# Kernel optimization log

Hardware: AMD Instinct MI355X
Metric: run time of the kernel (lower is better)

Reference implementation:

```python
import jax, jax.numpy as jnp
import numpy as np

NC = 16
NP_ = 2_000_000
Z_OFFSET = 50.0  # keep points well in front of every camera (stable 1/z)


def setup_inputs() -> dict:
    key = jax.random.key(0)
    k1, k2, k3, k4, k5 = jax.random.split(key, 5)
    pt3d = jax.random.normal(k1, (3, NP_), dtype=jnp.float32)
    R = jax.random.normal(k2, (NC, 3, 3), dtype=jnp.float32) * 0.3
    t = jax.random.normal(k3, (NC, 3), dtype=jnp.float32)
    t = t.at[:, 2].add(Z_OFFSET)
    f = jax.random.uniform(k4, (NC, 2), dtype=jnp.float32, minval=500.0, maxval=1500.0)
    c = jax.random.normal(k5, (NC, 2), dtype=jnp.float32) * 10.0
    mask = jnp.ones((NC, NP_), dtype=jnp.int32)  # full visibility (fixed output shape)
    return {"pt3d": pt3d, "R": R, "t": t, "f": f, "c": c, "mask": mask}


def reference(pt3d, R, t, f, c, mask):
    # Camera-frame points for every camera: Xc[n] = R[n] @ pt3d + t[n]  -> (Nc, 3, Np)
    Xc = jnp.einsum('nij,jp->nip', R, pt3d) + t[:, :, None]
    # Pinhole projection: (u, v) = f * (x/z, y/z) + c  -> (Nc, 2, Np)
    uv = Xc[:, :2, :] / Xc[:, 2:3, :] * f[:, :, None] + c[:, :, None]
    # Per-camera transpose to (Np, 2), then concat over cameras -> (Nc*Np, 2)
    return jnp.transpose(uv, (0, 2, 1)).reshape(-1, 2)
```

## Files before the change

kernel.cpp:

```cpp
#include <hip/hip_runtime.h>

#define NP 2000000
#define NC 16

typedef float vfloat4 __attribute__((ext_vector_type(4)));

__global__ __launch_bounds__(256) void Projection_19713899889207_kernel(
    const float* __restrict__ pt3d,
    const float* __restrict__ R,
    const float* __restrict__ t,
    const float* __restrict__ f,
    const float* __restrict__ c,
    float* __restrict__ out)
{
    int pair = blockIdx.x * blockDim.x + threadIdx.x;
    int p = pair * 2;
    if (p >= NP) return;

    float2 px = *(const float2*)(pt3d + 0 * NP + p);
    float2 py = *(const float2*)(pt3d + 1 * NP + p);
    float2 pz = *(const float2*)(pt3d + 2 * NP + p);

    for (int n = 0; n < NC; ++n) {
        const float* Rn = R + n * 9;
        float r00 = Rn[0], r01 = Rn[1], r02 = Rn[2];
        float r10 = Rn[3], r11 = Rn[4], r12 = Rn[5];
        float r20 = Rn[6], r21 = Rn[7], r22 = Rn[8];
        float t0 = t[n * 3 + 0], t1 = t[n * 3 + 1], t2 = t[n * 3 + 2];
        float fx = f[n * 2 + 0], fy = f[n * 2 + 1];
        float cx = c[n * 2 + 0], cy = c[n * 2 + 1];

        float X0 = r00 * px.x + r01 * py.x + r02 * pz.x + t0;
        float Y0 = r10 * px.x + r11 * py.x + r12 * pz.x + t1;
        float Z0 = r20 * px.x + r21 * py.x + r22 * pz.x + t2;
        float X1 = r00 * px.y + r01 * py.y + r02 * pz.y + t0;
        float Y1 = r10 * px.y + r11 * py.y + r12 * pz.y + t1;
        float Z1 = r20 * px.y + r21 * py.y + r22 * pz.y + t2;

        float iz0 = 1.0f / Z0;
        float iz1 = 1.0f / Z1;

        vfloat4 o;
        o.x = fx * X0 * iz0 + cx;
        o.y = fy * Y0 * iz0 + cy;
        o.z = fx * X1 * iz1 + cx;
        o.w = fy * Y1 * iz1 + cy;

        vfloat4* dst = (vfloat4*)(out + (size_t)n * (size_t)NP * 2 + (size_t)p * 2);
        __builtin_nontemporal_store(o, dst);
    }
}

extern "C" void kernel_launch(void* const* d_in, const int* in_sizes, int n_in,
                              void* d_out, int out_size, void* d_ws, size_t ws_size,
                              hipStream_t stream) {
    const float* pt3d = (const float*)d_in[0];
    const float* R    = (const float*)d_in[1];
    const float* t    = (const float*)d_in[2];
    const float* f    = (const float*)d_in[3];
    const float* c    = (const float*)d_in[4];
    float* out = (float*)d_out;

    int pairs = NP / 2;
    int blocks = (pairs + 255) / 256;
    Projection_19713899889207_kernel<<<blocks, 256, 0, stream>>>(pt3d, R, t, f, c, out);
}
```

Measured before the change: 336.5 us.

## Parallelize cameras across grid y and process four points per thread

Moves the per-camera loop into a 2D grid so each block handles one camera, with each thread projecting four points and issuing two contiguous 16-byte nontemporal stores. This is meant to increase parallelism and keep each block's writes contiguous instead of striding across 16 output regions. In exchange, the input point cloud is re-read once per camera, relying on cache to absorb the extra reads.

```diff
diff --git a/kernel.cpp b/kernel.cpp
--- a/kernel.cpp
+++ b/kernel.cpp
@@ -13,42 +13,42 @@
     const float* __restrict__ c,
     float* __restrict__ out)
 {
-    int pair = blockIdx.x * blockDim.x + threadIdx.x;
-    int p = pair * 2;
+    const int n   = blockIdx.y;
+    const int tid = blockIdx.x * blockDim.x + threadIdx.x;
+    const int p   = tid * 4;
     if (p >= NP) return;
 
-    float2 px = *(const float2*)(pt3d + 0 * NP + p);
-    float2 py = *(const float2*)(pt3d + 1 * NP + p);
-    float2 pz = *(const float2*)(pt3d + 2 * NP + p);
+    const float* Rn = R + n * 9;
+    const float r00 = Rn[0], r01 = Rn[1], r02 = Rn[2];
+    const float r10 = Rn[3], r11 = Rn[4], r12 = Rn[5];
+    const float r20 = Rn[6], r21 = Rn[7], r22 = Rn[8];
+    const float t0 = t[n * 3 + 0], t1 = t[n * 3 + 1], t2 = t[n * 3 + 2];
+    const float fx = f[n * 2 + 0], fy = f[n * 2 + 1];
+    const float cx = c[n * 2 + 0], cy = c[n * 2 + 1];
 
-    for (int n = 0; n < NC; ++n) {
-        const float* Rn = R + n * 9;
-        float r00 = Rn[0], r01 = Rn[1], r02 = Rn[2];
-        float r10 = Rn[3], r11 = Rn[4], r12 = Rn[5];
-        float r20 = Rn[6], r21 = Rn[7], r22 = Rn[8];
-        float t0 = t[n * 3 + 0], t1 = t[n * 3 + 1], t2 = t[n * 3 + 2];
-        float fx = f[n * 2 + 0], fy = f[n * 2 + 1];
-        float cx = c[n * 2 + 0], cy = c[n * 2 + 1];
+    const vfloat4 px = *(const vfloat4*)(pt3d + 0 * NP + p);
+    const vfloat4 py = *(const vfloat4*)(pt3d + 1 * NP + p);
+    const vfloat4 pz = *(const vfloat4*)(pt3d + 2 * NP + p);
 
-        float X0 = r00 * px.x + r01 * py.x + r02 * pz.x + t0;
-        float Y0 = r10 * px.x + r11 * py.x + r12 * pz.x + t1;
-        float Z0 = r20 * px.x + r21 * py.x + r22 * pz.x + t2;
-        float X1 = r00 * px.y + r01 * py.y + r02 * pz.y + t0;
-        float Y1 = r10 * px.y + r11 * py.y + r12 * pz.y + t1;
-        float Z1 = r20 * px.y + r21 * py.y + r22 * pz.y + t2;
+    float u[4], v[4];
+#pragma unroll
+    for (int k = 0; k < 4; ++k) {
+        const float x = px[k], y = py[k], z = pz[k];
+        const float X = r00 * x + r01 * y + r02 * z + t0;
+        const float Y = r10 * x + r11 * y + r12 * z + t1;
+        const float Z = r20 * x + r21 * y + r22 * z + t2;
+        const float iz = 1.0f / Z;
+        u[k] = fx * X * iz + cx;
+        v[k] = fy * Y * iz + cy;
+    }
 
-        float iz0 = 1.0f / Z0;
-        float iz1 = 1.0f / Z1;
+    vfloat4 o0, o1;
+    o0.x = u[0]; o0.y = v[0]; o0.z = u[1]; o0.w = v[1];
+    o1.x = u[2]; o1.y = v[2]; o1.z = u[3]; o1.w = v[3];
 
-        vfloat4 o;
-        o.x = fx * X0 * iz0 + cx;
-        o.y = fy * Y0 * iz0 + cy;
-        o.z = fx * X1 * iz1 + cx;
-        o.w = fy * Y1 * iz1 + cy;
-
-        vfloat4* dst = (vfloat4*)(out + (size_t)n * (size_t)NP * 2 + (size_t)p * 2);
-        __builtin_nontemporal_store(o, dst);
-    }
+    float* dst = out + (size_t)n * (size_t)NP * 2 + (size_t)p * 2;
+    __builtin_nontemporal_store(o0, (vfloat4*)(dst + 0));
+    __builtin_nontemporal_store(o1, (vfloat4*)(dst + 4));
 }
 
 extern "C" void kernel_launch(void* const* d_in, const int* in_sizes, int n_in,
@@ -61,7 +61,8 @@
     const float* c    = (const float*)d_in[4];
     float* out = (float*)d_out;
 
-    int pairs = NP / 2;
-    int blocks = (pairs + 255) / 256;
-    Projection_19713899889207_kernel<<<blocks, 256, 0, stream>>>(pt3d, R, t, f, c, out);
+    const int quads    = NP / 4;
+    const int blocks_x = (quads + 255) / 256;
+    dim3 grid(blocks_x, NC, 1);
+    Projection_19713899889207_kernel<<<grid, 256, 0, stream>>>(pt3d, R, t, f, c, out);
 }
```

Result: slower. 401.9 us (+19.4%).
